# Kernel tuning notes

Hardware: AMD Instinct MI355X
Metric: run time of the kernel (lower is better)

Reference implementation:

```python
import jax, jax.numpy as jnp
import numpy as np

B, UNITS, DIM = 8192, 2048, 32


def setup_inputs() -> dict:
    key = jax.random.key(0)
    kx, kc = jax.random.split(key)
    x = jax.random.normal(kx, (B, DIM), dtype=jnp.float32)
    # centers initialized with RandomUniform(0, 1) as in the keras layer
    centers = jax.random.uniform(kc, (UNITS, DIM), dtype=jnp.float32)
    gamma = jnp.ones((1,), dtype=jnp.float32)  # Constant(1.0), non-trainable
    return {"x": x, "centers": centers, "gamma": gamma}


def reference(x, centers, gamma):
    # diff: [B, units, dim] broadcasted, then sum of squares over dim -> [B, units]
    diff = x[:, None, :] - centers[None, :, :]
    sq_dist = jnp.sum(diff * diff, axis=-1)
    return jnp.exp(-gamma * sq_dist)  # gamma shape (1,) broadcasts
```

## Files before the change

kernel.cpp:

```cpp
#include <hip/hip_runtime.h>
#include <math.h>


#define BATCH   8192
#define UNITS   2048
#define DIM     32
#define BM      64
#define BN      128
#define THREADS 256
#define NXCD    8
#define ITERS   4

typedef __attribute__((ext_vector_type(8))) short s16x8;
typedef __attribute__((ext_vector_type(4))) float f32x4;

static __device__ __forceinline__ unsigned bf16_rne(float v) {
    unsigned u = __builtin_bit_cast(unsigned, v);
    return (u + 0x7FFFu + ((u >> 16) & 1u)) >> 16;
}

static __device__ __forceinline__ void load8(const float* __restrict__ p, float* v) {
    float4 t0 = *reinterpret_cast<const float4*>(p);
    float4 t1 = *reinterpret_cast<const float4*>(p + 4);
    v[0] = t0.x; v[1] = t0.y; v[2] = t0.z; v[3] = t0.w;
    v[4] = t1.x; v[5] = t1.y; v[6] = t1.z; v[7] = t1.w;
}

static __device__ __forceinline__ void split8(const float* v, s16x8& hi, s16x8& lo) {
#pragma unroll
    for (int j = 0; j < 8; ++j) {
        unsigned h = bf16_rne(v[j]);
        float hf = __builtin_bit_cast(float, h << 16);
        unsigned l = bf16_rne(v[j] - hf);
        hi[j] = (short)h;
        lo[j] = (short)l;
    }
}

__global__ __launch_bounds__(THREADS, 2) void rbf_stream(
    const float* __restrict__ x,
    const float* __restrict__ centers,
    const float* __restrict__ gamma,
    float* __restrict__ out)
{
    __shared__ __align__(16) f32x4 s_t[4][16][32];

    const int tid  = threadIdx.x;
    const int w    = tid >> 6;
    const int lane = tid & 63;
    const int l16  = lane & 15;
    const int kq   = lane >> 4;

    const int bid = blockIdx.x;
    const int xcd = bid & (NXCD - 1);
    const int rlo = bid >> 3;
    const int cb  = rlo & 15;
    const int sb  = rlo >> 4;
    const int c0  = cb * BN;

    const float kg = -gamma[0] * 1.4426950408889634f;
    const float m2 = -2.0f * kg;

    s16x8 b_hi[8], b_lo[8];
    float kgcnq[8][4];
#pragma unroll
    for (int n = 0; n < 8; ++n) {
        float v[8];
        load8(centers + (size_t)(c0 + n * 16 + l16) * DIM + kq * 8, v);
        split8(v, b_hi[n], b_lo[n]);
        float pn = 0.f;
#pragma unroll
        for (int j = 0; j < 8; ++j) pn = fmaf(v[j], v[j], pn);
        pn += __shfl_xor(pn, 16);
        pn += __shfl_xor(pn, 32);
#pragma unroll
        for (int j = 0; j < 4; ++j)
            kgcnq[n][j] = kg * __shfl(pn, kq * 4 + j);
    }

    float xf[2][8];
    load8(x + (size_t)((xcd * 16 + sb) * BM + w * 16 + l16) * DIM + kq * 8, xf[0]);

#pragma unroll
    for (int k = 0; k < ITERS; ++k) {
        const int cur = k & 1;
        const int r0  = (xcd * 16 + k * 4 + sb) * BM;

        if (k + 1 < ITERS) {
            const int r1 = (xcd * 16 + (k + 1) * 4 + sb) * BM;
            load8(x + (size_t)(r1 + w * 16 + l16) * DIM + kq * 8, xf[cur ^ 1]);
        }

        s16x8 a_hi, a_lo;
        split8(xf[cur], a_hi, a_lo);
        float pn = 0.f;
#pragma unroll
        for (int j = 0; j < 8; ++j) pn = fmaf(xf[cur][j], xf[cur][j], pn);
        pn += __shfl_xor(pn, 16);
        pn += __shfl_xor(pn, 32);
        const float kgxn = kg * pn;

#pragma unroll
        for (int n = 0; n < 8; ++n) {
            f32x4 acc = {0.f, 0.f, 0.f, 0.f};
            acc = __builtin_amdgcn_mfma_f32_16x16x32_bf16(b_lo[n], a_hi, acc, 0, 0, 0);
            acc = __builtin_amdgcn_mfma_f32_16x16x32_bf16(b_hi[n], a_lo, acc, 0, 0, 0);
            acc = __builtin_amdgcn_mfma_f32_16x16x32_bf16(b_hi[n], a_hi, acc, 0, 0, 0);

            f32x4 o;
            o[0] = __builtin_amdgcn_exp2f(fmaf(m2, acc[0], kgxn + kgcnq[n][0]));
            o[1] = __builtin_amdgcn_exp2f(fmaf(m2, acc[1], kgxn + kgcnq[n][1]));
            o[2] = __builtin_amdgcn_exp2f(fmaf(m2, acc[2], kgxn + kgcnq[n][2]));
            o[3] = __builtin_amdgcn_exp2f(fmaf(m2, acc[3], kgxn + kgcnq[n][3]));

            const int s = ((n * 4 + kq) + l16 * 4) & 31;
            s_t[w][l16][s] = o;
        }

#pragma unroll
        for (int p = 0; p < 8; ++p) {
            const int row = 2 * p + (lane >> 5);
            const int sl  = ((lane & 31) + row * 4) & 31;
            f32x4 v = s_t[w][row][sl];
            float* op = out + (size_t)(r0 + w * 16 + row) * UNITS
                            + c0 + (lane & 31) * 4;
            *reinterpret_cast<f32x4*>(op) = v;
        }
    }
}

extern "C" void kernel_launch(void* const* d_in, const int* in_sizes, int n_in,
                              void* d_out, int out_size, void* d_ws, size_t ws_size,
                              hipStream_t stream)
{
    const float* x       = (const float*)d_in[0];
    const float* centers = (const float*)d_in[1];
    const float* gamma   = (const float*)d_in[2];
    float* out           = (float*)d_out;

    dim3 grid(512);
    dim3 block(THREADS);
    rbf_stream<<<grid, block, 0, stream>>>(x, centers, gamma, out);
}
```

Baseline: 22.15 us.

## Drop LDS transpose staging, store MFMA results directly, halve column tile

Removes the shared-memory transpose used to produce 512-byte contiguous row stores. Each lane now writes its float4 from the MFMA accumulator straight to global memory, so each row gets 64-byte segments. The column tile drops from 128 to 64 and the grid doubles to 1024 blocks, with launch bounds raised to 4 blocks per CU to increase occupancy. The trade is fewer LDS round-trips and more parallelism against less coalesced global stores for a write-bound output.

```diff
diff --git a/kernel.cpp b/kernel.cpp
--- a/kernel.cpp
+++ b/kernel.cpp
@@ -6,7 +6,7 @@
 #define UNITS   2048
 #define DIM     32
 #define BM      64
-#define BN      128
+#define BN      64
 #define THREADS 256
 #define NXCD    8
 #define ITERS   4
@@ -37,34 +37,32 @@
     }
 }
 
-__global__ __launch_bounds__(THREADS, 2) void rbf_stream(
+__global__ __launch_bounds__(THREADS, 4) void rbf_stream(
     const float* __restrict__ x,
     const float* __restrict__ centers,
     const float* __restrict__ gamma,
     float* __restrict__ out)
 {
-    __shared__ __align__(16) f32x4 s_t[4][16][32];
-
     const int tid  = threadIdx.x;
     const int w    = tid >> 6;
     const int lane = tid & 63;
     const int l16  = lane & 15;
     const int kq   = lane >> 4;
 
-    const int bid = blockIdx.x;
-    const int xcd = bid & (NXCD - 1);
-    const int rlo = bid >> 3;
-    const int cb  = rlo & 15;
-    const int sb  = rlo >> 4;
-    const int c0  = cb * BN;
+    const int bid  = blockIdx.x;
+    const int xcd  = bid & (NXCD - 1);
+    const int rest = bid >> 3;
+    const int cb   = rest & 31;
+    const int sb   = rest >> 5;
+    const int c0   = cb * BN;
 
     const float kg = -gamma[0] * 1.4426950408889634f;
     const float m2 = -2.0f * kg;
 
-    s16x8 b_hi[8], b_lo[8];
-    float kgcnq[8][4];
+    s16x8 b_hi[4], b_lo[4];
+    float kgcnq[4][4];
 #pragma unroll
-    for (int n = 0; n < 8; ++n) {
+    for (int n = 0; n < 4; ++n) {
         float v[8];
         load8(centers + (size_t)(c0 + n * 16 + l16) * DIM + kq * 8, v);
         split8(v, b_hi[n], b_lo[n]);
@@ -101,30 +99,21 @@
         const float kgxn = kg * pn;
 
 #pragma unroll
-        for (int n = 0; n < 8; ++n) {
+        for (int n = 0; n < 4; ++n) {
             f32x4 acc = {0.f, 0.f, 0.f, 0.f};
             acc = __builtin_amdgcn_mfma_f32_16x16x32_bf16(b_lo[n], a_hi, acc, 0, 0, 0);
             acc = __builtin_amdgcn_mfma_f32_16x16x32_bf16(b_hi[n], a_lo, acc, 0, 0, 0);
             acc = __builtin_amdgcn_mfma_f32_16x16x32_bf16(b_hi[n], a_hi, acc, 0, 0, 0);
 
-            f32x4 o;
-            o[0] = __builtin_amdgcn_exp2f(fmaf(m2, acc[0], kgxn + kgcnq[n][0]));
-            o[1] = __builtin_amdgcn_exp2f(fmaf(m2, acc[1], kgxn + kgcnq[n][1]));
-            o[2] = __builtin_amdgcn_exp2f(fmaf(m2, acc[2], kgxn + kgcnq[n][2]));
-            o[3] = __builtin_amdgcn_exp2f(fmaf(m2, acc[3], kgxn + kgcnq[n][3]));
+            float4 o;
+            o.x = __builtin_amdgcn_exp2f(fmaf(m2, acc[0], kgxn + kgcnq[n][0]));
+            o.y = __builtin_amdgcn_exp2f(fmaf(m2, acc[1], kgxn + kgcnq[n][1]));
+            o.z = __builtin_amdgcn_exp2f(fmaf(m2, acc[2], kgxn + kgcnq[n][2]));
+            o.w = __builtin_amdgcn_exp2f(fmaf(m2, acc[3], kgxn + kgcnq[n][3]));
 
-            const int s = ((n * 4 + kq) + l16 * 4) & 31;
-            s_t[w][l16][s] = o;
-        }
-
-#pragma unroll
-        for (int p = 0; p < 8; ++p) {
-            const int row = 2 * p + (lane >> 5);
-            const int sl  = ((lane & 31) + row * 4) & 31;
-            f32x4 v = s_t[w][row][sl];
-            float* op = out + (size_t)(r0 + w * 16 + row) * UNITS
-                            + c0 + (lane & 31) * 4;
-            *reinterpret_cast<f32x4*>(op) = v;
+            float* op = out + (size_t)(r0 + w * 16 + l16) * UNITS
+                            + (c0 + n * 16 + kq * 4);
+            *reinterpret_cast<float4*>(op) = o;
         }
     }
 }
@@ -138,7 +127,7 @@
     const float* gamma   = (const float*)d_in[2];
     float* out           = (float*)d_out;
 
-    dim3 grid(512);
+    dim3 grid(1024);
     dim3 block(THREADS);
     rbf_stream<<<grid, block, 0, stream>>>(x, centers, gamma, out);
 }
```

After: 21.79 us. About the same (-1.6%).
